# Kernel optimization log

Hardware: AMD Instinct MI355X
Metric: run time of the kernel (lower is better)

The kernel has to match this reference:

```python
import jax, jax.numpy as jnp
import numpy as np
from jax import lax

V, E, H = 32000, 512, 512
B, S = 64, 64


def _lstm_cell(x, h, c, wih, whh, b):
    # PyTorch gate order: i, f, g, o
    g = x @ wih.T + h @ whh.T + b
    i, f, gg, o = jnp.split(g, 4, axis=-1)
    c2 = jax.nn.sigmoid(f) * c + jax.nn.sigmoid(i) * jnp.tanh(gg)
    h2 = jax.nn.sigmoid(o) * jnp.tanh(c2)
    return h2, c2


def setup_inputs() -> dict:
    key = jax.random.key(0)
    ks = jax.random.split(key, 16)
    s = 0.05
    return {
        "hidden_state": jax.random.normal(ks[0], (4, B, H), jnp.float32) * s,
        "cell_state": jax.random.normal(ks[1], (4, B, H), jnp.float32) * s,
        "Y": jax.random.randint(ks[2], (B, S), 0, V),
        "emb": jax.random.normal(ks[3], (V, E), jnp.float32) * s,
        "w_ih_l0": jax.random.normal(ks[4], (2, 4 * H, E), jnp.float32) * s,
        "w_hh_l0": jax.random.normal(ks[5], (2, 4 * H, H), jnp.float32) * s,
        "b_ih_l0": jax.random.normal(ks[6], (2, 4 * H), jnp.float32) * s,
        "b_hh_l0": jax.random.normal(ks[7], (2, 4 * H), jnp.float32) * s,
        "w_ih_l1": jax.random.normal(ks[8], (2, 4 * H, 2 * H), jnp.float32) * s,
        "w_hh_l1": jax.random.normal(ks[9], (2, 4 * H, H), jnp.float32) * s,
        "b_ih_l1": jax.random.normal(ks[10], (2, 4 * H), jnp.float32) * s,
        "b_hh_l1": jax.random.normal(ks[11], (2, 4 * H), jnp.float32) * s,
        "fc_w": jax.random.normal(ks[12], (V, 2 * H), jnp.float32) * s,
        "fc_b": jax.random.normal(ks[13], (V,), jnp.float32) * s,
    }


def reference(hidden_state, cell_state, Y, emb, w_ih_l0, w_hh_l0, b_ih_l0,
              b_hh_l0, w_ih_l1, w_hh_l1, b_ih_l1, b_hh_l1, fc_w, fc_b):
    # Deterministic teacher-forcing: input at step 0 is Y[:,1]; at step i>0 it is Y[:,i-1].
    idx_seq = jnp.concatenate([Y[:, 1:2], Y[:, :-1]], axis=1)  # (B,S)
    xs = idx_seq.T  # (S,B)
    b0 = b_ih_l0 + b_hh_l0  # (2,4H)
    b1 = b_ih_l1 + b_hh_l1

    def step(carry, idx):
        h, c = carry  # (4,B,H): [l0_fwd, l0_bwd, l1_fwd, l1_bwd]
        x = emb[idx]  # (B,E)
        h0f, c0f = _lstm_cell(x, h[0], c[0], w_ih_l0[0], w_hh_l0[0], b0[0])
        h0b, c0b = _lstm_cell(x, h[1], c[1], w_ih_l0[1], w_hh_l0[1], b0[1])
        x1 = jnp.concatenate([h0f, h0b], axis=-1)  # (B,2H)
        h1f, c1f = _lstm_cell(x1, h[2], c[2], w_ih_l1[0], w_hh_l1[0], b1[0])
        h1b, c1b = _lstm_cell(x1, h[3], c[3], w_ih_l1[1], w_hh_l1[1], b1[1])
        out = jnp.concatenate([h1f, h1b], axis=-1)  # (B,2H)
        h2 = jnp.stack([h0f, h0b, h1f, h1b])
        c2 = jnp.stack([c0f, c0b, c1f, c1b])
        return (h2, c2), out

    (_, _), outs = lax.scan(step, (hidden_state, cell_state), xs)  # (S,B,2H)
    logits = outs @ fc_w.T + fc_b  # (S,B,V)
    # permute to (B,S,V) then flatten, as in the torch code
    return jnp.transpose(logits, (1, 0, 2)).reshape(-1, fc_w.shape[0])
```

## Files before the change

### kernel.cpp

```cpp
#include <hip/hip_runtime.h>
#include <hip/hip_bf16.h>
#include <stdint.h>

#define S_ 64
#define B_ 64
#define E_ 512
#define H_ 512
#define V_ 32000
#define G4 2048
#define SB 4096

#define OROW_US 64000
#define GTAIL_US 59904

typedef __attribute__((ext_vector_type(8))) short short8;
typedef __attribute__((ext_vector_type(4))) float f32x4;
typedef __attribute__((ext_vector_type(4))) int i32x4;

static __device__ __forceinline__ unsigned short f2bf(float f) {
  unsigned u = __float_as_uint(f);
  u += 0x7fff + ((u >> 16) & 1);
  return (unsigned short)(u >> 16);
}
static __device__ __forceinline__ unsigned pk2(float a, float b) {
  return (unsigned)f2bf(a) | ((unsigned)f2bf(b) << 16);
}
static __device__ __forceinline__ float bf2f(unsigned short u) {
  return __uint_as_float((unsigned)u << 16);
}
static __device__ __forceinline__ float sigm(float x) {
  return 1.f / (1.f + expf(-x));
}

__device__ __forceinline__ void gload_lds16(const void* g, void* l) {
  __builtin_amdgcn_global_load_lds(
      (const __attribute__((address_space(1))) void*)g,
      (__attribute__((address_space(3))) void*)l, 16, 0, 0);
}

__device__ __forceinline__ void st128_sys(void* p, i32x4 v) {
  asm volatile("global_store_dwordx4 %0, %1, off sc0 sc1"
               :: "v"((unsigned long long)p), "v"(v) : "memory");
}
__device__ __forceinline__ void wait_vm0() {
  asm volatile("s_waitcnt vmcnt(0)" ::: "memory");
}

__device__ __forceinline__ void spin_ge(unsigned* c, unsigned tgt) {
  while (__hip_atomic_load(c, __ATOMIC_RELAXED, __HIP_MEMORY_SCOPE_AGENT) < tgt)
    __builtin_amdgcn_s_sleep(1);
}
__device__ __forceinline__ void arrive(unsigned* c) {
  __hip_atomic_fetch_add(c, 1u, __ATOMIC_RELAXED, __HIP_MEMORY_SCOPE_AGENT);
}

#define CIDX(t, d, p) ((((t) * 8) + ((d) * 4) + (p)) * 64)
#define CNT_BYTES (64 * 8 * 64 * 4)

__global__ void k_f2bf4(const float* __restrict__ s0, const float* __restrict__ s1,
                        const float* __restrict__ s2, const float* __restrict__ s3,
                        unsigned short* __restrict__ dst) {
  const int c0 = 2 * G4 * E_ / 8, c1 = c0 + 2 * G4 * H_ / 8,
            c2 = c1 + 2 * G4 * 1024 / 8, c3 = c2 + 2 * G4 * H_ / 8;
  int i8 = blockIdx.x * blockDim.x + threadIdx.x;
  int stride = gridDim.x * blockDim.x;
  for (; i8 < c3; i8 += stride) {
    const float* s; int o8;
    if (i8 < c0) { s = s0; o8 = i8; }
    else if (i8 < c1) { s = s1; o8 = i8 - c0; }
    else if (i8 < c2) { s = s2; o8 = i8 - c1; }
    else { s = s3; o8 = i8 - c2; }
    int o = o8 * 8;
    float4 x = *(const float4*)&s[o];
    float4 y = *(const float4*)&s[o + 4];
    i32x4 v = {(int)pk2(x.x, x.y), (int)pk2(x.z, x.w),
               (int)pk2(y.x, y.y), (int)pk2(y.z, y.w)};
    *(i32x4*)&dst[i8 * 8] = v;
  }
}

__global__ void k_f2bf(const float* __restrict__ in, unsigned short* __restrict__ out, int n) {
  int i = blockIdx.x * blockDim.x + threadIdx.x;
  int stride = gridDim.x * blockDim.x;
  for (; i < n; i += stride) out[i] = f2bf(in[i]);
}

__global__ void k_addbias(const float* __restrict__ a, const float* __restrict__ b,
                          float* __restrict__ out, int n) {
  int i = blockIdx.x * blockDim.x + threadIdx.x;
  if (i < n) out[i] = a[i] + b[i];
}

__global__ void k_gather(const int* __restrict__ Y, const float* __restrict__ emb,
                         unsigned short* __restrict__ X) {
  int sb = blockIdx.x;
  int t = sb >> 6, b = sb & 63;
  int idx = (t == 0) ? Y[b * S_ + 1] : Y[b * S_ + t - 1];
  const float* src = emb + (size_t)idx * E_;
  unsigned short* dst = X + (size_t)sb * E_;
  for (int e = threadIdx.x; e < E_; e += blockDim.x) dst[e] = f2bf(src[e]);
}

__global__ void k_init_h(const float* __restrict__ hid,
                         unsigned short* __restrict__ h0i, unsigned short* __restrict__ h1i) {
  int i = blockIdx.x * blockDim.x + threadIdx.x;
  if (i >= 4 * B_ * H_) return;
  unsigned short v = f2bf(hid[i]);
  if (i < 2 * B_ * H_) h0i[i] = v;
  else h1i[i - 2 * B_ * H_] = v;
}

__global__ __launch_bounds__(256) void k_gemm_g0(
    const unsigned short* __restrict__ A, const unsigned short* __restrict__ B,
    const float* __restrict__ bias, unsigned short* __restrict__ C,
    int K, int nTM, int nwg) {
  __shared__ unsigned short Als[128 * 32];
  __shared__ unsigned short Bls[128 * 32];
  int tid = threadIdx.x;
  int o = blockIdx.x;
  int wg = (o & 7) * (nwg >> 3) + (o >> 3);
  int bm = wg % nTM, bn = wg / nTM;
  int w = tid >> 6, l = tid & 63;
  int wr = w >> 1, wc = w & 1;
  int lr = l & 15, hi = l >> 4;
  int c0 = w * 128 + l;
  int row0 = c0 >> 2, ks0 = (((c0 & 3) ^ (row0 & 3)) * 8);
  int c1 = c0 + 64;
  int row1 = c1 >> 2, ks1 = (((c1 & 3) ^ (row1 & 3)) * 8);
  const unsigned short* Ab = A + (size_t)(bm * 128) * K;
  const unsigned short* Bb = B + (size_t)(bn * 128) * K;
  unsigned short* AlsW = &Als[w * 1024];
  unsigned short* BlsW = &Bls[w * 1024];
  int co = ((hi ^ (lr & 3)) * 8);
  f32x4 acc[4][4] = {};
  for (int kk = 0; kk < K; kk += 32) {
    __syncthreads();
    gload_lds16(Ab + (size_t)row0 * K + kk + ks0, AlsW);
    gload_lds16(Ab + (size_t)row1 * K + kk + ks1, AlsW + 512);
    gload_lds16(Bb + (size_t)row0 * K + kk + ks0, BlsW);
    gload_lds16(Bb + (size_t)row1 * K + kk + ks1, BlsW + 512);
    __syncthreads();
    short8 af[4], bfr[4];
#pragma unroll
    for (int r = 0; r < 4; r++)
      af[r] = *(const short8*)&Als[(wr * 64 + r * 16 + lr) * 32 + co];
#pragma unroll
    for (int c4 = 0; c4 < 4; c4++)
      bfr[c4] = *(const short8*)&Bls[(wc * 64 + c4 * 16 + lr) * 32 + co];
#pragma unroll
    for (int r = 0; r < 4; r++)
#pragma unroll
      for (int c4 = 0; c4 < 4; c4++)
        acc[r][c4] = __builtin_amdgcn_mfma_f32_16x16x32_bf16(af[r], bfr[c4], acc[r][c4], 0, 0, 0);
  }
  int rbase = bm * 128 + wr * 64 + hi * 4;
  int cbase = bn * 128 + wc * 64 + lr;
#pragma unroll
  for (int r = 0; r < 4; r++) {
#pragma unroll
    for (int c4 = 0; c4 < 4; c4++) {
      int cc = cbase + c4 * 16;
      float bv = bias[cc];
#pragma unroll
      for (int j = 0; j < 4; j++) {
        int rr = rbase + r * 16 + j;
        C[(size_t)rr * OROW_US + GTAIL_US + cc] = f2bf(acc[r][c4][j] + bv);
      }
    }
  }
}

__global__ __launch_bounds__(256) void k_gemm_fc(
    const unsigned short* __restrict__ A, const unsigned short* __restrict__ B,
    const float* __restrict__ bias, float* __restrict__ C,
    int N, int K, int nTM, int nwg) {
  __shared__ unsigned short Als[128 * 32];
  __shared__ unsigned short Bls[128 * 32];
  int tid = threadIdx.x;
  int o = blockIdx.x;
  int wg = (o & 7) * (nwg >> 3) + (o >> 3);
  int bm = wg % nTM, bn = wg / nTM;
  int w = tid >> 6, l = tid & 63;
  int wr = w >> 1, wc = w & 1;
  int lr = l & 15, hi = l >> 4;
  int c0 = w * 128 + l;
  int row0 = c0 >> 2, ks0 = (((c0 & 3) ^ (row0 & 3)) * 8);
  int c1 = c0 + 64;
  int row1 = c1 >> 2, ks1 = (((c1 & 3) ^ (row1 & 3)) * 8);
  const unsigned short* Ab = A + (size_t)(bm * 128) * K;
  const unsigned short* Bb = B + (size_t)(bn * 128) * K;
  unsigned short* AlsW = &Als[w * 1024];
  unsigned short* BlsW = &Bls[w * 1024];
  int co = ((hi ^ (lr & 3)) * 8);
  f32x4 acc[4][4] = {};
  for (int kk = 0; kk < K; kk += 32) {
    __syncthreads();
    gload_lds16(Ab + (size_t)row0 * K + kk + ks0, AlsW);
    gload_lds16(Ab + (size_t)row1 * K + kk + ks1, AlsW + 512);
    gload_lds16(Bb + (size_t)row0 * K + kk + ks0, BlsW);
    gload_lds16(Bb + (size_t)row1 * K + kk + ks1, BlsW + 512);
    __syncthreads();
    short8 af[4], bfr[4];
#pragma unroll
    for (int r = 0; r < 4; r++)
      af[r] = *(const short8*)&Als[(wr * 64 + r * 16 + lr) * 32 + co];
#pragma unroll
    for (int c4 = 0; c4 < 4; c4++)
      bfr[c4] = *(const short8*)&Bls[(wc * 64 + c4 * 16 + lr) * 32 + co];
#pragma unroll
    for (int r = 0; r < 4; r++)
#pragma unroll
      for (int c4 = 0; c4 < 4; c4++)
        acc[r][c4] = __builtin_amdgcn_mfma_f32_16x16x32_bf16(af[r], bfr[c4], acc[r][c4], 0, 0, 0);
  }
  int rbase = bm * 128 + wr * 64 + hi * 4;
  int cbase = bn * 128 + wc * 64 + lr;
#pragma unroll
  for (int r = 0; r < 4; r++) {
#pragma unroll
    for (int c4 = 0; c4 < 4; c4++) {
      int cc = cbase + c4 * 16;
      float bv = bias[cc];
#pragma unroll
      for (int j = 0; j < 4; j++) {
        int rr = rbase + r * 16 + j;
        size_t orow = (size_t)((rr & 63) * 64 + (rr >> 6));
        __builtin_nontemporal_store(acc[r][c4][j] + bv, &C[orow * (size_t)N + cc]);
      }
    }
  }
}

#define LDW0 520
#define LDW1 1544
#define NBLK 192

__global__ __launch_bounds__(256) void k_fused_lstm(
    const unsigned short* __restrict__ h0i,
    const unsigned short* __restrict__ h1i,
    const float* __restrict__ cell,
    const unsigned short* __restrict__ whh0,
    const unsigned short* __restrict__ wih1,
    const unsigned short* __restrict__ whh1,
    const float* __restrict__ b1s,
    const unsigned short* __restrict__ G0u,
    unsigned short* __restrict__ H0,
    unsigned short* __restrict__ O1,
    unsigned* __restrict__ cnt0, unsigned* __restrict__ cnt1) {
  __shared__ unsigned short SM[32 * LDW1];
  __shared__ __align__(16) unsigned short HS[64 * 16];
  int tid = threadIdx.x;
  int w = tid >> 6, l = tid & 63;
  int lr = l & 15, hi = l >> 4;

  if (blockIdx.x < 64) {
    int d = blockIdx.x >> 5, jt = blockIdx.x & 31;
    const unsigned short* Wd = whh0 + (size_t)d * (G4 * H_);
    for (int c = tid; c < 64 * 64; c += 256) {
      int row = c >> 6, ck = c & 63;
      int g = row >> 4, r16 = row & 15;
      *(int4*)&SM[row * LDW0 + ck * 8] =
          *(const int4*)&Wd[(size_t)(g * H_ + jt * 16 + r16) * H_ + ck * 8];
    }
    int j = jt * 16 + lr;
    int b0 = w * 16 + hi * 4;
    f32x4 creg;
    {
      const float* cd = cell + (size_t)d * (B_ * H_);
#pragma unroll
      for (int jj = 0; jj < 4; jj++) creg[jj] = cd[(size_t)(b0 + jj) * H_ + j];
    }
    __syncthreads();
    float gv[4][4];
    auto preloadG = [&](int t) {
#pragma unroll
      for (int jj = 0; jj < 4; jj++) {
        const unsigned short* Gb =
            G0u + (size_t)(t * B_ + b0 + jj) * OROW_US + GTAIL_US + d * 2048 + j;
#pragma unroll
        for (int g = 0; g < 4; g++) gv[g][jj] = bf2f(Gb[g * 512]);
      }
    };
    preloadG(0);
    for (int t = 0; t < S_; ++t) {
      if (t >= 1) {
        if (tid < 4) spin_ge(&cnt0[CIDX(t - 1, d, tid)], 8);
        __syncthreads();
      }
      const unsigned short* hp = (t == 0) ? h0i + (size_t)d * (B_ * H_)
                                          : H0 + (size_t)(t - 1) * B_ * 1024 + d * 512;
      size_t hstr = (t == 0) ? (size_t)H_ : 1024;
      const unsigned short* arow = hp + (size_t)(w * 16 + lr) * hstr + hi * 8;
      f32x4 acc[4] = {};
#pragma unroll
      for (int ki = 0; ki < 16; ki++) {
        short8 a = *(const short8*)&arow[ki * 32];
#pragma unroll
        for (int g = 0; g < 4; g++) {
          short8 bfr = *(const short8*)&SM[(g * 16 + lr) * LDW0 + ki * 32 + hi * 8];
          acc[g] = __builtin_amdgcn_mfma_f32_16x16x32_bf16(a, bfr, acc[g], 0, 0, 0);
        }
      }
#pragma unroll
      for (int jj = 0; jj < 4; jj++) {
        float gi = acc[0][jj] + gv[0][jj];
        float gf = acc[1][jj] + gv[1][jj];
        float gg = acc[2][jj] + gv[2][jj];
        float go = acc[3][jj] + gv[3][jj];
        float c = sigm(gf) * creg[jj] + sigm(gi) * tanhf(gg);
        creg[jj] = c;
        HS[(b0 + jj) * 16 + lr] = f2bf(sigm(go) * tanhf(c));
      }
      __syncthreads();
      unsigned short* Ho = H0 + (size_t)t * B_ * 1024 + d * 512 + jt * 16;
      if (tid < 128) {
        int r = tid >> 1, half = tid & 1;
        st128_sys(&Ho[(size_t)r * 1024 + half * 8], *(const i32x4*)&HS[r * 16 + half * 8]);
      }
      wait_vm0();
      __syncthreads();
      if (tid == 0) arrive(&cnt0[CIDX(t, d, jt & 3)]);
      if (t + 1 < S_) preloadG(t + 1);
    }
  } else {
    int idx = blockIdx.x - 64;
    int d = idx >> 6, jt8 = idx & 63;
    int j0 = jt8 * 8;
    {
      const unsigned short* Wih = wih1 + (size_t)d * (G4 * 1024);
      const unsigned short* Whh = whh1 + (size_t)d * (G4 * H_);
      for (int c = tid; c < 32 * 192; c += 256) {
        int r = c / 192, ck = c - r * 192;
        int g = r >> 3, jc = r & 7;
        const unsigned short* src =
            (ck < 128) ? Wih + (size_t)(g * H_ + j0 + jc) * 1024 + ck * 8
                       : Whh + (size_t)(g * H_ + j0 + jc) * H_ + (ck - 128) * 8;
        *(int4*)&SM[r * LDW1 + ck * 8] = *(const int4*)src;
      }
    }
    int j = j0 + (lr & 7);
    const float* b1d = b1s + d * G4;
    float bi_ = b1d[j], bf_ = b1d[512 + j], bg_ = b1d[1024 + j], bo_ = b1d[1536 + j];
    int b0 = w * 16 + hi * 4;
    f32x4 creg = {};
    if (lr < 8) {
      const float* cd = cell + (size_t)(2 + d) * (B_ * H_);
#pragma unroll
      for (int jj = 0; jj < 4; jj++) creg[jj] = cd[(size_t)(b0 + jj) * H_ + j];
    }
    __syncthreads();

    f32x4 acc0, acc1;
    {
      if (tid < 8) spin_ge(&cnt0[CIDX(0, 0, 0) + tid * 64], 8);
      __syncthreads();
      acc0 = (f32x4){}; acc1 = (f32x4){};
      const unsigned short* x1row = H0 + ((size_t)0 * B_ + w * 16 + lr) * 1024 + hi * 8;
#pragma unroll 8
      for (int ki = 0; ki < 32; ki++) {
        short8 a = *(const short8*)&x1row[ki * 32];
        short8 bA = *(const short8*)&SM[(size_t)lr * LDW1 + ki * 32 + hi * 8];
        short8 bB = *(const short8*)&SM[(size_t)(16 + lr) * LDW1 + ki * 32 + hi * 8];
        acc0 = __builtin_amdgcn_mfma_f32_16x16x32_bf16(a, bA, acc0, 0, 0, 0);
        acc1 = __builtin_amdgcn_mfma_f32_16x16x32_bf16(a, bB, acc1, 0, 0, 0);
      }
    }
    for (int t = 0; t < S_; ++t) {
      if (t >= 1) {
        if (tid < 4) spin_ge(&cnt1[CIDX(t - 1, d, tid)], 16);
        __syncthreads();
      }
      const unsigned short* hprev = (t == 0)
          ? h1i + (size_t)d * (B_ * H_) + (size_t)(w * 16 + lr) * H_ + hi * 8
          : O1 + ((size_t)(t - 1) * B_ + w * 16 + lr) * 1024 + d * 512 + hi * 8;
#pragma unroll 8
      for (int ki = 0; ki < 16; ki++) {
        short8 a = *(const short8*)&hprev[ki * 32];
        short8 bA = *(const short8*)&SM[(size_t)lr * LDW1 + 1024 + ki * 32 + hi * 8];
        short8 bB = *(const short8*)&SM[(size_t)(16 + lr) * LDW1 + 1024 + ki * 32 + hi * 8];
        acc0 = __builtin_amdgcn_mfma_f32_16x16x32_bf16(a, bA, acc0, 0, 0, 0);
        acc1 = __builtin_amdgcn_mfma_f32_16x16x32_bf16(a, bB, acc1, 0, 0, 0);
      }
      float pf[4], po[4];
#pragma unroll
      for (int jj = 0; jj < 4; jj++) {
        pf[jj] = __shfl_xor(acc0[jj], 8);
        po[jj] = __shfl_xor(acc1[jj], 8);
      }
      if (lr < 8) {
#pragma unroll
        for (int jj = 0; jj < 4; jj++) {
          float gi = acc0[jj] + bi_;
          float gf = pf[jj] + bf_;
          float gg = acc1[jj] + bg_;
          float go = po[jj] + bo_;
          float c = sigm(gf) * creg[jj] + sigm(gi) * tanhf(gg);
          creg[jj] = c;
          HS[(b0 + jj) * 8 + lr] = f2bf(sigm(go) * tanhf(c));
        }
      }
      __syncthreads();
      unsigned short* Oo = O1 + (size_t)t * B_ * 1024 + d * 512 + j0;
      if (tid < 64) st128_sys(&Oo[(size_t)tid * 1024], *(const i32x4*)&HS[tid * 8]);
      wait_vm0();
      __syncthreads();
      if (tid == 0 && t + 1 < S_) arrive(&cnt1[CIDX(t, d, jt8 & 3)]);
      if (t + 1 < S_) {
        if (tid < 8) spin_ge(&cnt0[CIDX(t + 1, 0, 0) + tid * 64], 8);
        __syncthreads();
        acc0 = (f32x4){}; acc1 = (f32x4){};
        const unsigned short* x1row =
            H0 + ((size_t)(t + 1) * B_ + w * 16 + lr) * 1024 + hi * 8;
#pragma unroll 8
        for (int ki = 0; ki < 32; ki++) {
          short8 a = *(const short8*)&x1row[ki * 32];
          short8 bA = *(const short8*)&SM[(size_t)lr * LDW1 + ki * 32 + hi * 8];
          short8 bB = *(const short8*)&SM[(size_t)(16 + lr) * LDW1 + ki * 32 + hi * 8];
          acc0 = __builtin_amdgcn_mfma_f32_16x16x32_bf16(a, bA, acc0, 0, 0, 0);
          acc1 = __builtin_amdgcn_mfma_f32_16x16x32_bf16(a, bB, acc1, 0, 0, 0);
        }
      }
    }
  }
}

extern "C" void kernel_launch(void* const* d_in, const int* in_sizes, int n_in,
                              void* d_out, int out_size, void* d_ws, size_t ws_size,
                              hipStream_t stream) {
  const float* hidden = (const float*)d_in[0];
  const float* cell   = (const float*)d_in[1];
  const int*   Y      = (const int*)d_in[2];
  const float* emb    = (const float*)d_in[3];
  const float* wih0   = (const float*)d_in[4];
  const float* whh0   = (const float*)d_in[5];
  const float* bih0   = (const float*)d_in[6];
  const float* bhh0   = (const float*)d_in[7];
  const float* wih1   = (const float*)d_in[8];
  const float* whh1   = (const float*)d_in[9];
  const float* bih1   = (const float*)d_in[10];
  const float* bhh1   = (const float*)d_in[11];
  const float* fcw    = (const float*)d_in[12];
  const float* fcb    = (const float*)d_in[13];

  char* ws = (char*)d_ws;
  size_t off = 0;
  auto alloc = [&](size_t bytes) {
    void* p = ws + off;
    off += (bytes + 255) & ~(size_t)255;
    return p;
  };
  unsigned short* wih0b = (unsigned short*)alloc((size_t)2 * G4 * E_ * 2);
  unsigned short* whh0b = (unsigned short*)alloc((size_t)2 * G4 * H_ * 2);
  unsigned short* wih1b = (unsigned short*)alloc((size_t)2 * G4 * 1024 * 2);
  unsigned short* whh1b = (unsigned short*)alloc((size_t)2 * G4 * H_ * 2);
  unsigned short* fcwb  = (unsigned short*)alloc((size_t)V_ * 1024 * 2);
  unsigned short* Xb    = (unsigned short*)alloc((size_t)SB * E_ * 2);
  unsigned short* H0    = (unsigned short*)alloc((size_t)SB * 1024 * 2);
  unsigned short* O1    = (unsigned short*)alloc((size_t)SB * 1024 * 2);
  unsigned short* h0i   = (unsigned short*)alloc((size_t)2 * B_ * H_ * 2);
  unsigned short* h1i   = (unsigned short*)alloc((size_t)2 * B_ * H_ * 2);
  float* b0s = (float*)alloc((size_t)2 * G4 * 4);
  float* b1s = (float*)alloc((size_t)2 * G4 * 4);
  unsigned* cnt0 = (unsigned*)alloc(CNT_BYTES);
  unsigned* cnt1 = (unsigned*)alloc(CNT_BYTES);
  (void)ws_size;

  k_f2bf4<<<2048, 256, 0, stream>>>(wih0, whh0, wih1, whh1, wih0b);
  k_f2bf<<<4096, 256, 0, stream>>>(fcw, fcwb, V_ * 1024);
  k_addbias<<<16, 256, 0, stream>>>(bih0, bhh0, b0s, 2 * G4);
  k_addbias<<<16, 256, 0, stream>>>(bih1, bhh1, b1s, 2 * G4);
  k_gather<<<SB, 256, 0, stream>>>(Y, emb, Xb);
  k_init_h<<<512, 256, 0, stream>>>(hidden, h0i, h1i);
  (void)hipMemsetAsync(cnt0, 0, CNT_BYTES, stream);
  (void)hipMemsetAsync(cnt1, 0, CNT_BYTES, stream);

  k_gemm_g0<<<1024, 256, 0, stream>>>(Xb, wih0b, b0s, (unsigned short*)d_out,
                                      E_, SB / 128, 1024);

  k_fused_lstm<<<NBLK, 256, 0, stream>>>(h0i, h1i, cell, whh0b, wih1b, whh1b,
                                         b1s, (const unsigned short*)d_out,
                                         H0, O1, cnt0, cnt1);

  k_gemm_fc<<<(SB / 128) * (V_ / 128), 256, 0, stream>>>(
      O1, fcwb, fcb, (float*)d_out, V_, 1024, SB / 128, (SB / 128) * (V_ / 128));
}
```

Baseline: 1.186 ms.

## Repartition fused LSTM into 64 larger blocks with 512 threads each

The persistent fused LSTM kernel drops from 192 blocks of 256 threads to 64 blocks of 512 threads, each owning 32 hidden units across all four gates. Layer-1 blocks now keep only the recurrent weights in LDS and stream the input-to-hidden weights from global/L2 each step. This removes the cross-lane gate shuffle and cuts the number of blocks that must arrive at each per-step counter, so each barrier waits on fewer participants. In exchange there is less parallelism across CUs and more global traffic for the layer-1 input projection on every step.

```diff
diff --git a/kernel.cpp b/kernel.cpp
--- a/kernel.cpp
+++ b/kernel.cpp
@@ -231,11 +231,10 @@
   }
 }
 
-#define LDW0 520
-#define LDW1 1544
-#define NBLK 192
-
-__global__ __launch_bounds__(256) void k_fused_lstm(
+#define LDWr 520
+#define NBLK 64
+
+__global__ __launch_bounds__(512) void k_fused_lstm(
     const unsigned short* __restrict__ h0i,
     const unsigned short* __restrict__ h1i,
     const float* __restrict__ cell,
@@ -247,30 +246,38 @@
     unsigned short* __restrict__ H0,
     unsigned short* __restrict__ O1,
     unsigned* __restrict__ cnt0, unsigned* __restrict__ cnt1) {
-  __shared__ unsigned short SM[32 * LDW1];
-  __shared__ __align__(16) unsigned short HS[64 * 16];
+  __shared__ unsigned short SM[128 * LDWr];
+  __shared__ __align__(16) unsigned short HS[64 * 32];
   int tid = threadIdx.x;
   int w = tid >> 6, l = tid & 63;
   int lr = l & 15, hi = l >> 4;
-
-  if (blockIdx.x < 64) {
-    int d = blockIdx.x >> 5, jt = blockIdx.x & 31;
-    const unsigned short* Wd = whh0 + (size_t)d * (G4 * H_);
-    for (int c = tid; c < 64 * 64; c += 256) {
+  int bt = w >> 1, jc = w & 1;
+
+  bool isL0 = blockIdx.x < 32;
+  int idx = isL0 ? blockIdx.x : blockIdx.x - 32;
+  int d = idx >> 4, jt = idx & 15;
+  int j0 = jt * 32;
+
+  {
+    const unsigned short* Wd = (isL0 ? whh0 : whh1) + (size_t)d * (G4 * H_);
+    for (int c = tid; c < 128 * 64; c += 512) {
       int row = c >> 6, ck = c & 63;
-      int g = row >> 4, r16 = row & 15;
-      *(int4*)&SM[row * LDW0 + ck * 8] =
-          *(const int4*)&Wd[(size_t)(g * H_ + jt * 16 + r16) * H_ + ck * 8];
+      int g = row >> 5, rr = row & 31;
+      *(int4*)&SM[row * LDWr + ck * 8] =
+          *(const int4*)&Wd[(size_t)(g * H_ + j0 + rr) * H_ + ck * 8];
     }
-    int j = jt * 16 + lr;
-    int b0 = w * 16 + hi * 4;
-    f32x4 creg;
-    {
-      const float* cd = cell + (size_t)d * (B_ * H_);
-#pragma unroll
-      for (int jj = 0; jj < 4; jj++) creg[jj] = cd[(size_t)(b0 + jj) * H_ + j];
-    }
-    __syncthreads();
+  }
+  int j = j0 + jc * 16 + lr;
+  int b0 = bt * 16 + hi * 4;
+  f32x4 creg;
+  {
+    const float* cd = cell + (size_t)((isL0 ? 0 : 2) + d) * (B_ * H_);
+#pragma unroll
+    for (int jj = 0; jj < 4; jj++) creg[jj] = cd[(size_t)(b0 + jj) * H_ + j];
+  }
+  __syncthreads();
+
+  if (isL0) {
     float gv[4][4];
     auto preloadG = [&](int t) {
 #pragma unroll
@@ -284,20 +291,20 @@
     preloadG(0);
     for (int t = 0; t < S_; ++t) {
       if (t >= 1) {
-        if (tid < 4) spin_ge(&cnt0[CIDX(t - 1, d, tid)], 8);
+        if (tid == 0) spin_ge(&cnt0[CIDX(t - 1, d, 0)], 16);
         __syncthreads();
       }
       const unsigned short* hp = (t == 0) ? h0i + (size_t)d * (B_ * H_)
                                           : H0 + (size_t)(t - 1) * B_ * 1024 + d * 512;
       size_t hstr = (t == 0) ? (size_t)H_ : 1024;
-      const unsigned short* arow = hp + (size_t)(w * 16 + lr) * hstr + hi * 8;
+      const unsigned short* arow = hp + (size_t)(bt * 16 + lr) * hstr + hi * 8;
       f32x4 acc[4] = {};
 #pragma unroll
       for (int ki = 0; ki < 16; ki++) {
         short8 a = *(const short8*)&arow[ki * 32];
 #pragma unroll
         for (int g = 0; g < 4; g++) {
-          short8 bfr = *(const short8*)&SM[(g * 16 + lr) * LDW0 + ki * 32 + hi * 8];
+          short8 bfr = *(const short8*)&SM[(g * 32 + jc * 16 + lr) * LDWr + ki * 32 + hi * 8];
           acc[g] = __builtin_amdgcn_mfma_f32_16x16x32_bf16(a, bfr, acc[g], 0, 0, 0);
         }
       }
@@ -309,117 +316,84 @@
         float go = acc[3][jj] + gv[3][jj];
         float c = sigm(gf) * creg[jj] + sigm(gi) * tanhf(gg);
         creg[jj] = c;
-        HS[(b0 + jj) * 16 + lr] = f2bf(sigm(go) * tanhf(c));
+        HS[(b0 + jj) * 32 + jc * 16 + lr] = f2bf(sigm(go) * tanhf(c));
       }
       __syncthreads();
-      unsigned short* Ho = H0 + (size_t)t * B_ * 1024 + d * 512 + jt * 16;
-      if (tid < 128) {
-        int r = tid >> 1, half = tid & 1;
-        st128_sys(&Ho[(size_t)r * 1024 + half * 8], *(const i32x4*)&HS[r * 16 + half * 8]);
+      unsigned short* Ho = H0 + (size_t)t * B_ * 1024 + d * 512 + j0;
+      if (tid < 256) {
+        int r = tid >> 2, q = tid & 3;
+        st128_sys(&Ho[(size_t)r * 1024 + q * 8], *(const i32x4*)&HS[r * 32 + q * 8]);
       }
       wait_vm0();
       __syncthreads();
-      if (tid == 0) arrive(&cnt0[CIDX(t, d, jt & 3)]);
+      if (tid == 0) arrive(&cnt0[CIDX(t, d, 0)]);
       if (t + 1 < S_) preloadG(t + 1);
     }
   } else {
-    int idx = blockIdx.x - 64;
-    int d = idx >> 6, jt8 = idx & 63;
-    int j0 = jt8 * 8;
-    {
-      const unsigned short* Wih = wih1 + (size_t)d * (G4 * 1024);
-      const unsigned short* Whh = whh1 + (size_t)d * (G4 * H_);
-      for (int c = tid; c < 32 * 192; c += 256) {
-        int r = c / 192, ck = c - r * 192;
-        int g = r >> 3, jc = r & 7;
-        const unsigned short* src =
-            (ck < 128) ? Wih + (size_t)(g * H_ + j0 + jc) * 1024 + ck * 8
-                       : Whh + (size_t)(g * H_ + j0 + jc) * H_ + (ck - 128) * 8;
-        *(int4*)&SM[r * LDW1 + ck * 8] = *(const int4*)src;
-      }
-    }
-    int j = j0 + (lr & 7);
     const float* b1d = b1s + d * G4;
-    float bi_ = b1d[j], bf_ = b1d[512 + j], bg_ = b1d[1024 + j], bo_ = b1d[1536 + j];
-    int b0 = w * 16 + hi * 4;
-    f32x4 creg = {};
-    if (lr < 8) {
-      const float* cd = cell + (size_t)(2 + d) * (B_ * H_);
-#pragma unroll
-      for (int jj = 0; jj < 4; jj++) creg[jj] = cd[(size_t)(b0 + jj) * H_ + j];
-    }
-    __syncthreads();
-
-    f32x4 acc0, acc1;
-    {
-      if (tid < 8) spin_ge(&cnt0[CIDX(0, 0, 0) + tid * 64], 8);
+    float bi_[4];
+#pragma unroll
+    for (int g = 0; g < 4; g++) bi_[g] = b1d[g * 512 + j];
+    const unsigned short* Wg[4];
+#pragma unroll
+    for (int g = 0; g < 4; g++)
+      Wg[g] = wih1 + (size_t)d * (G4 * 1024) +
+              (size_t)(g * 512 + j0 + jc * 16 + lr) * 1024 + hi * 8;
+    f32x4 acc[4];
+    auto x1phase = [&](int t) {
+      if (tid < 2) spin_ge(&cnt0[CIDX(t, tid, 0)], 16);
       __syncthreads();
-      acc0 = (f32x4){}; acc1 = (f32x4){};
-      const unsigned short* x1row = H0 + ((size_t)0 * B_ + w * 16 + lr) * 1024 + hi * 8;
-#pragma unroll 8
+#pragma unroll
+      for (int g = 0; g < 4; g++) acc[g] = (f32x4){};
+      const unsigned short* x1row = H0 + ((size_t)t * B_ + bt * 16 + lr) * 1024 + hi * 8;
+#pragma unroll 4
       for (int ki = 0; ki < 32; ki++) {
         short8 a = *(const short8*)&x1row[ki * 32];
-        short8 bA = *(const short8*)&SM[(size_t)lr * LDW1 + ki * 32 + hi * 8];
-        short8 bB = *(const short8*)&SM[(size_t)(16 + lr) * LDW1 + ki * 32 + hi * 8];
-        acc0 = __builtin_amdgcn_mfma_f32_16x16x32_bf16(a, bA, acc0, 0, 0, 0);
-        acc1 = __builtin_amdgcn_mfma_f32_16x16x32_bf16(a, bB, acc1, 0, 0, 0);
-      }
-    }
+#pragma unroll
+        for (int g = 0; g < 4; g++) {
+          short8 bfr = *(const short8*)&Wg[g][ki * 32];
+          acc[g] = __builtin_amdgcn_mfma_f32_16x16x32_bf16(a, bfr, acc[g], 0, 0, 0);
+        }
+      }
+    };
+    x1phase(0);
     for (int t = 0; t < S_; ++t) {
       if (t >= 1) {
-        if (tid < 4) spin_ge(&cnt1[CIDX(t - 1, d, tid)], 16);
+        if (tid == 0) spin_ge(&cnt1[CIDX(t - 1, d, 0)], 16);
         __syncthreads();
       }
       const unsigned short* hprev = (t == 0)
-          ? h1i + (size_t)d * (B_ * H_) + (size_t)(w * 16 + lr) * H_ + hi * 8
-          : O1 + ((size_t)(t - 1) * B_ + w * 16 + lr) * 1024 + d * 512 + hi * 8;
-#pragma unroll 8
+          ? h1i + (size_t)d * (B_ * H_) + (size_t)(bt * 16 + lr) * H_ + hi * 8
+          : O1 + ((size_t)(t - 1) * B_ + bt * 16 + lr) * 1024 + d * 512 + hi * 8;
+#pragma unroll
       for (int ki = 0; ki < 16; ki++) {
         short8 a = *(const short8*)&hprev[ki * 32];
-        short8 bA = *(const short8*)&SM[(size_t)lr * LDW1 + 1024 + ki * 32 + hi * 8];
-        short8 bB = *(const short8*)&SM[(size_t)(16 + lr) * LDW1 + 1024 + ki * 32 + hi * 8];
-        acc0 = __builtin_amdgcn_mfma_f32_16x16x32_bf16(a, bA, acc0, 0, 0, 0);
-        acc1 = __builtin_amdgcn_mfma_f32_16x16x32_bf16(a, bB, acc1, 0, 0, 0);
-      }
-      float pf[4], po[4];
+#pragma unroll
+        for (int g = 0; g < 4; g++) {
+          short8 bfr = *(const short8*)&SM[(g * 32 + jc * 16 + lr) * LDWr + ki * 32 + hi * 8];
+          acc[g] = __builtin_amdgcn_mfma_f32_16x16x32_bf16(a, bfr, acc[g], 0, 0, 0);
+        }
+      }
 #pragma unroll
       for (int jj = 0; jj < 4; jj++) {
-        pf[jj] = __shfl_xor(acc0[jj], 8);
-        po[jj] = __shfl_xor(acc1[jj], 8);
-      }
-      if (lr < 8) {
-#pragma unroll
-        for (int jj = 0; jj < 4; jj++) {
-          float gi = acc0[jj] + bi_;
-          float gf = pf[jj] + bf_;
-          float gg = acc1[jj] + bg_;
-          float go = po[jj] + bo_;
-          float c = sigm(gf) * creg[jj] + sigm(gi) * tanhf(gg);
-          creg[jj] = c;
-          HS[(b0 + jj) * 8 + lr] = f2bf(sigm(go) * tanhf(c));
-        }
+        float gi = acc[0][jj] + bi_[0];
+        float gf = acc[1][jj] + bi_[1];
+        float gg = acc[2][jj] + bi_[2];
+        float go = acc[3][jj] + bi_[3];
+        float c = sigm(gf) * creg[jj] + sigm(gi) * tanhf(gg);
+        creg[jj] = c;
+        HS[(b0 + jj) * 32 + jc * 16 + lr] = f2bf(sigm(go) * tanhf(c));
       }
       __syncthreads();
       unsigned short* Oo = O1 + (size_t)t * B_ * 1024 + d * 512 + j0;
-      if (tid < 64) st128_sys(&Oo[(size_t)tid * 1024], *(const i32x4*)&HS[tid * 8]);
+      if (tid < 256) {
+        int r = tid >> 2, q = tid & 3;
+        st128_sys(&Oo[(size_t)r * 1024 + q * 8], *(const i32x4*)&HS[r * 32 + q * 8]);
+      }
       wait_vm0();
       __syncthreads();
-      if (tid == 0 && t + 1 < S_) arrive(&cnt1[CIDX(t, d, jt8 & 3)]);
-      if (t + 1 < S_) {
-        if (tid < 8) spin_ge(&cnt0[CIDX(t + 1, 0, 0) + tid * 64], 8);
-        __syncthreads();
-        acc0 = (f32x4){}; acc1 = (f32x4){};
-        const unsigned short* x1row =
-            H0 + ((size_t)(t + 1) * B_ + w * 16 + lr) * 1024 + hi * 8;
-#pragma unroll 8
-        for (int ki = 0; ki < 32; ki++) {
-          short8 a = *(const short8*)&x1row[ki * 32];
-          short8 bA = *(const short8*)&SM[(size_t)lr * LDW1 + ki * 32 + hi * 8];
-          short8 bB = *(const short8*)&SM[(size_t)(16 + lr) * LDW1 + ki * 32 + hi * 8];
-          acc0 = __builtin_amdgcn_mfma_f32_16x16x32_bf16(a, bA, acc0, 0, 0, 0);
-          acc1 = __builtin_amdgcn_mfma_f32_16x16x32_bf16(a, bB, acc1, 0, 0, 0);
-        }
-      }
+      if (tid == 0 && t + 1 < S_) arrive(&cnt1[CIDX(t, d, 0)]);
+      if (t + 1 < S_) x1phase(t + 1);
     }
   }
 }
@@ -477,7 +451,7 @@
   k_gemm_g0<<<1024, 256, 0, stream>>>(Xb, wih0b, b0s, (unsigned short*)d_out,
                                       E_, SB / 128, 1024);
 
-  k_fused_lstm<<<NBLK, 256, 0, stream>>>(h0i, h1i, cell, whh0b, wih1b, whh1b,
+  k_fused_lstm<<<NBLK, 512, 0, stream>>>(h0i, h1i, cell, whh0b, wih1b, whh1b,
                                          b1s, (const unsigned short*)d_out,
                                          H0, O1, cnt0, cnt1);
 
```

New measurement: 3.138 ms. 2.65x slower.
